# Kernel tuning notes

Measured on AMD Instinct MI355X. Metric: run time of the kernel, lower is better.

The kernel has to match this reference:

```python
import jax, jax.numpy as jnp
import numpy as np

DIM = 768
HEADS = 12
HEAD_DIM = DIM // HEADS
EPS_ATTN = 1e-6
LN_EPS = 1e-5


def _piece_weight():
    # BlockDistanceConv with num_patches_per_side=16, patch_group_size=16 -> 4x4 blocks
    bps = 4
    centers = np.array([[i + 0.5, j + 0.5] for i in range(bps) for j in range(bps)], dtype=np.float32)
    d = np.linalg.norm(centers[:, None, :] - centers[None, :, :], axis=-1)
    mat = np.cos(d / d.max() * np.pi / 4.0)  # 'cos' transform
    mat = mat / mat.sum(axis=0, keepdims=True)
    return jnp.asarray(mat, dtype=jnp.float32)  # [16, 16], out = W @ x over piece channels


def setup_inputs() -> dict:
    key = jax.random.key(0)
    ks = jax.random.split(key, 4)
    B, N, W, C = 128, 16, 16, DIM
    x = jax.random.normal(ks[0], (B, N, W, C), dtype=jnp.float32)
    ln_gamma = jnp.ones((C,), dtype=jnp.float32)
    ln_beta = jnp.zeros((C,), dtype=jnp.float32)
    w_qkv = jax.random.normal(ks[1], (C, 3 * C), dtype=jnp.float32) * (C ** -0.5)
    w_out = jax.random.normal(ks[2], (C, C), dtype=jnp.float32) * (C ** -0.5)
    b_out = jnp.zeros((C,), dtype=jnp.float32)
    w_piece = _piece_weight()
    return {"x": x, "ln_gamma": ln_gamma, "ln_beta": ln_beta, "w_qkv": w_qkv,
            "w_out": w_out, "b_out": b_out, "w_piece": w_piece}


def reference(x, ln_gamma, ln_beta, w_qkv, w_out, b_out, w_piece):
    B, N, W, C = x.shape
    H, D = HEADS, HEAD_DIM
    # LayerNorm over channel dim
    mu = jnp.mean(x, axis=-1, keepdims=True)
    var = jnp.mean((x - mu) ** 2, axis=-1, keepdims=True)
    xn = (x - mu) * jax.lax.rsqrt(var + LN_EPS) * ln_gamma + ln_beta
    # qkv projection (no bias)
    qkv = xn @ w_qkv  # [B,N,W,3C]
    q, k, v = jnp.split(qkv, 3, axis=-1)
    # relu kernel feature map
    q = jax.nn.relu(q) + EPS_ATTN
    k = jax.nn.relu(k) + EPS_ATTN
    # split heads: 'b n w (h d) -> b h n w d'
    def heads(t):
        return t.reshape(B, N, W, H, D).transpose(0, 3, 1, 2, 4)
    q, k, v = heads(q), heads(k), heads(v)
    # per-window kv = k^T v  (sum over window positions w)  -> [B,H,N,D,D]
    kv = jnp.einsum('bhnwd,bhnwe->bhnde', k, v)
    # BlockDistanceConv: 1x1 conv mixing over piece dim N with fixed weights
    kv = jnp.einsum('ij,bhjde->bhide', w_piece, kv)
    # out = q @ kv  -> [B,H,N,W,D]
    out = jnp.einsum('bhnwd,bhnde->bhnwe', q, kv)
    # merge heads: 'b h n w d -> b n w (h d)'
    out = out.transpose(0, 2, 3, 1, 4).reshape(B, N, W, H * D)
    # output projection (dropout is identity in eval)
    return out @ w_out + b_out
```

## Files before the change

### kernel.cpp

```cpp
#include <hip/hip_runtime.h>

#define DIM 768
#define HEADS 12
#define TOK 32768

typedef unsigned short ushort_t;
typedef __attribute__((ext_vector_type(8))) short short8v;
typedef __attribute__((ext_vector_type(4))) float f32x4;
typedef __attribute__((ext_vector_type(4))) unsigned short us4;

__device__ __forceinline__ ushort_t f2bf(float x) {
  union { float f; unsigned u; } c; c.f = x;
  unsigned r = (c.u + 0x7FFFu + ((c.u >> 16) & 1u)) >> 16;
  return (ushort_t)r;
}

__device__ __forceinline__ void gload_lds16(const void* g, void* l) {
  __builtin_amdgcn_global_load_lds((const __attribute__((address_space(1))) void*)g,
                                   (__attribute__((address_space(3))) void*)l, 16, 0, 0);
}

__global__ __launch_bounds__(256) void ln_kernel(const float* __restrict__ x,
                                                 const float* __restrict__ g,
                                                 const float* __restrict__ be,
                                                 ushort_t* __restrict__ xn) {
  int t = blockIdx.x;
  int tid = threadIdx.x;
  const float* row = x + (size_t)t * DIM;
  float v0 = row[tid], v1 = row[tid + 256], v2 = row[tid + 512];
  float s  = v0 + v1 + v2;
  float sq = v0 * v0 + v1 * v1 + v2 * v2;
  #pragma unroll
  for (int off = 32; off; off >>= 1) {
    s  += __shfl_down(s, off);
    sq += __shfl_down(sq, off);
  }
  __shared__ float ls[4], lq[4];
  int wid = tid >> 6, lane = tid & 63;
  if (lane == 0) { ls[wid] = s; lq[wid] = sq; }
  __syncthreads();
  s  = ls[0] + ls[1] + ls[2] + ls[3];
  sq = lq[0] + lq[1] + lq[2] + lq[3];
  float mu  = s * (1.0f / DIM);
  float var = sq * (1.0f / DIM) - mu * mu;
  float rs  = rsqrtf(var + 1e-5f);
  ushort_t* orow = xn + (size_t)t * DIM;
  orow[tid]       = f2bf((v0 - mu) * rs * g[tid]       + be[tid]);
  orow[tid + 256] = f2bf((v1 - mu) * rs * g[tid + 256] + be[tid + 256]);
  orow[tid + 512] = f2bf((v2 - mu) * rs * g[tid + 512] + be[tid + 512]);
}

__global__ __launch_bounds__(256) void convT(const float* __restrict__ src,
                                             ushort_t* __restrict__ dst, int R, int Ccol) {
  __shared__ float tile[32][33];
  int c0 = blockIdx.x * 32, r0 = blockIdx.y * 32;
  int tx = threadIdx.x & 31, ty = threadIdx.x >> 5;
  #pragma unroll
  for (int i = 0; i < 32; i += 8)
    tile[ty + i][tx] = src[(size_t)(r0 + ty + i) * Ccol + c0 + tx];
  __syncthreads();
  #pragma unroll
  for (int i = 0; i < 32; i += 8)
    dst[(size_t)(c0 + ty + i) * R + r0 + tx] = f2bf(tile[tx][ty + i]);
}

template <int MODE>
__global__ __launch_bounds__(512, 2) void gemm_big(const ushort_t* __restrict__ A,
                                                   const ushort_t* __restrict__ Bt,
                                                   ushort_t* __restrict__ qbf,
                                                   ushort_t* __restrict__ kbf,
                                                   ushort_t* __restrict__ vTbf,
                                                   const float* __restrict__ bias,
                                                   float* __restrict__ C) {
  extern __shared__ __align__(16) char lds[];
  const int K = DIM, Kb = DIM * 2;
  const int N = (MODE == 0) ? 3 * DIM : DIM;
  const int nbn = N / 256;
  const int NT = K / 32;

  int bid = blockIdx.x;
  int qd = gridDim.x >> 3;
  int wid = (bid & 7) * qd + (bid >> 3);
  int bm = wid / nbn, bn = wid % nbn;
  int row0 = bm * 256, col0 = bn * 256;
  int t = threadIdx.x;
  int lane = t & 63, wave = t >> 6;
  int wr = wave >> 2, wcol = wave & 3;

  const char* Ag = (const char*)(A + (size_t)row0 * K);
  const char* Bg = (const char*)(Bt + (size_t)col0 * K);

  int o0 = t * 16, o1 = 8192 + t * 16;
  int ra0 = o0 >> 6, ra1 = o1 >> 6;
  int cb0 = (o0 & 63) ^ ((ra0 & 3) << 4);
  int cb1 = (o1 & 63) ^ ((ra1 & 3) << 4);
  size_t ga0 = (size_t)ra0 * Kb + cb0;
  size_t ga1 = (size_t)ra1 * Kb + cb1;

  int fr = lane & 15, fkb = (lane >> 4) << 4;
  int sw = fkb ^ ((fr & 3) << 4);
  int aoff = (wr * 128 + fr) * 64 + sw;
  int boff = 16384 + (wcol * 64 + fr) * 64 + sw;

  #define STAGE(tile, slot)                                            \
    do {                                                               \
      char* sb = lds + ((slot) * 32768);                               \
      size_t kb_ = (size_t)(tile) * 64;                                \
      gload_lds16(Ag + ga0 + kb_, sb + o0);                            \
      gload_lds16(Ag + ga1 + kb_, sb + o1);                            \
      gload_lds16(Bg + ga0 + kb_, sb + 16384 + o0);                    \
      gload_lds16(Bg + ga1 + kb_, sb + 16384 + o1);                    \
    } while (0)

  STAGE(0, 0);
  STAGE(1, 1);

  f32x4 acc[8][4] = {};
  for (int kt = 0; kt < NT; ++kt) {
    if (kt + 2 < NT) {
      STAGE(kt + 2, (kt + 2) & 3);
      asm volatile("s_waitcnt vmcnt(8)" ::: "memory");
    } else if (kt + 2 == NT) {
      asm volatile("s_waitcnt vmcnt(4)" ::: "memory");
    } else {
      asm volatile("s_waitcnt vmcnt(0)" ::: "memory");
    }
    __builtin_amdgcn_s_barrier();
    const char* As = lds + ((kt & 3) * 32768);
    short8v a[8], b[4];
    #pragma unroll
    for (int m = 0; m < 8; ++m) a[m] = *(const short8v*)(As + aoff + m * 1024);
    #pragma unroll
    for (int n = 0; n < 4; ++n) b[n] = *(const short8v*)(As + boff + n * 1024);
    __builtin_amdgcn_s_setprio(1);
    #pragma unroll
    for (int m = 0; m < 8; ++m)
      #pragma unroll
      for (int n = 0; n < 4; ++n)
        acc[m][n] = __builtin_amdgcn_mfma_f32_16x16x32_bf16(a[m], b[n], acc[m][n], 0, 0, 0);
    __builtin_amdgcn_s_setprio(0);
  }
  #undef STAGE

  int rbase = row0 + wr * 128 + ((lane >> 4) << 2);
  int cbase = col0 + wcol * 64 + fr;
  if constexpr (MODE == 0) {
    #pragma unroll
    for (int m = 0; m < 8; ++m) {
      int r0r = rbase + m * 16;
      #pragma unroll
      for (int n = 0; n < 4; ++n) {
        int c = cbase + n * 16;
        if (c < DIM) {
          #pragma unroll
          for (int j = 0; j < 4; ++j)
            qbf[(size_t)(r0r + j) * DIM + c] = f2bf(fmaxf(acc[m][n][j], 0.0f) + 1e-6f);
        } else if (c < 2 * DIM) {
          #pragma unroll
          for (int j = 0; j < 4; ++j)
            kbf[(size_t)(r0r + j) * DIM + (c - DIM)] = f2bf(fmaxf(acc[m][n][j], 0.0f) + 1e-6f);
        } else {
          int ch = c - 2 * DIM;
          int hh = ch >> 6, e = ch & 63;
          int bb = r0r >> 8, rr = r0r & 255;
          us4 pk;
          #pragma unroll
          for (int j = 0; j < 4; ++j) pk[j] = f2bf(acc[m][n][j]);
          *(us4*)&vTbf[((((size_t)bb * HEADS + hh) * 64 + e) << 8) + rr] = pk;
        }
      }
    }
  } else {
    #pragma unroll
    for (int m = 0; m < 8; ++m) {
      #pragma unroll
      for (int n = 0; n < 4; ++n) {
        int c = cbase + n * 16;
        float bz = bias[c];
        #pragma unroll
        for (int j = 0; j < 4; ++j)
          C[(size_t)(rbase + m * 16 + j) * N + c] = acc[m][n][j] + bz;
      }
    }
  }
}

__global__ __launch_bounds__(512) void attn_fused(const ushort_t* __restrict__ qbf,
                                                  const ushort_t* __restrict__ kbf,
                                                  const ushort_t* __restrict__ vTbf,
                                                  const float* __restrict__ wp,
                                                  ushort_t* __restrict__ attnO) {
  __shared__ __align__(16) char lds[65536];
  int bh = blockIdx.x;
  int b = bh / HEADS, h = bh % HEADS;
  int t = threadIdx.x;
  int lane = t & 63, wave = t >> 6;
  int wr = wave >> 2, wc = wave & 3;
  int fr = lane & 15, fkb = (lane >> 4) << 4;

  const char* qg = (const char*)(qbf + ((size_t)b * 256) * DIM + h * 64);
  const char* kg = (const char*)(kbf + ((size_t)b * 256) * DIM + h * 64);
  const char* vg = (const char*)(vTbf + ((size_t)bh << 14));

  for (int q4 = 0; q4 < 4; ++q4) {
    #pragma unroll
    for (int is = 0; is < 4; ++is) {
      int o = is * 8192 + t * 16;
      int r = o >> 7;
      int byt = (o & 127) ^ ((r & 7) << 4);
      gload_lds16(kg + (size_t)r * (DIM * 2) + byt, lds + o);
    }
    {
      int o = t * 16;
      int r = o >> 7;
      int byt = (o & 127) ^ ((r & 7) << 4);
      gload_lds16(qg + (size_t)(q4 * 64 + r) * (DIM * 2) + byt, lds + 32768 + o);
    }
    __syncthreads();
    f32x4 accA[2][4] = {};
    {
      short8v af[2][2], bfv[4][2];
      #pragma unroll
      for (int mt = 0; mt < 2; ++mt)
        #pragma unroll
        for (int ks = 0; ks < 2; ++ks) {
          int r = wr * 32 + mt * 16 + fr;
          int kb = ks * 64 + fkb;
          af[mt][ks] = *(const short8v*)(lds + 32768 + r * 128 + (kb ^ ((r & 7) << 4)));
        }
      #pragma unroll
      for (int nt = 0; nt < 4; ++nt)
        #pragma unroll
        for (int ks = 0; ks < 2; ++ks) {
          int c = wc * 64 + nt * 16 + fr;
          int kb = ks * 64 + fkb;
          bfv[nt][ks] = *(const short8v*)(lds + c * 128 + (kb ^ ((c & 7) << 4)));
        }
      #pragma unroll
      for (int mt = 0; mt < 2; ++mt)
        #pragma unroll
        for (int nt = 0; nt < 4; ++nt)
          #pragma unroll
          for (int ks = 0; ks < 2; ++ks)
            accA[mt][nt] = __builtin_amdgcn_mfma_f32_16x16x32_bf16(af[mt][ks], bfv[nt][ks],
                                                                   accA[mt][nt], 0, 0, 0);
    }
    ushort_t sv[2][4][4];
    #pragma unroll
    for (int mt = 0; mt < 2; ++mt)
      #pragma unroll
      for (int nt = 0; nt < 4; ++nt) {
        float wpf = wp[(q4 * 4 + wr * 2 + mt) * 16 + (wc * 4 + nt)];
        #pragma unroll
        for (int j = 0; j < 4; ++j) sv[mt][nt][j] = f2bf(accA[mt][nt][j] * wpf);
      }
    __syncthreads();
    #pragma unroll
    for (int mt = 0; mt < 2; ++mt)
      #pragma unroll
      for (int nt = 0; nt < 4; ++nt)
        #pragma unroll
        for (int j = 0; j < 4; ++j) {
          int rs = wr * 32 + mt * 16 + ((lane >> 4) << 2) + j;
          int cs = wc * 64 + nt * 16 + fr;
          *(ushort_t*)(lds + 32768 + rs * 512 + ((cs * 2) ^ ((rs & 7) << 4))) = sv[mt][nt][j];
        }
    #pragma unroll
    for (int is = 0; is < 4; ++is) {
      int o = is * 8192 + t * 16;
      int e = o >> 9;
      int byt = (o & 511) ^ ((e & 7) << 4);
      gload_lds16(vg + e * 512 + byt, lds + o);
    }
    __syncthreads();
    f32x4 accB[2] = {{0.f,0.f,0.f,0.f},{0.f,0.f,0.f,0.f}};
    #pragma unroll
    for (int ks = 0; ks < 8; ++ks) {
      int kb = ks * 64 + fkb;
      int e = wc * 16 + fr;
      short8v bv = *(const short8v*)(lds + e * 512 + (kb ^ ((e & 7) << 4)));
      #pragma unroll
      for (int mt = 0; mt < 2; ++mt) {
        int r = wr * 32 + mt * 16 + fr;
        short8v av = *(const short8v*)(lds + 32768 + r * 512 + (kb ^ ((r & 7) << 4)));
        accB[mt] = __builtin_amdgcn_mfma_f32_16x16x32_bf16(av, bv, accB[mt], 0, 0, 0);
      }
    }
    #pragma unroll
    for (int mt = 0; mt < 2; ++mt) {
      int row = b * 256 + q4 * 64 + wr * 32 + mt * 16 + ((lane >> 4) << 2);
      int col = h * 64 + wc * 16 + fr;
      #pragma unroll
      for (int j = 0; j < 4; ++j)
        attnO[(size_t)(row + j) * DIM + col] = f2bf(accB[mt][j]);
    }
    __syncthreads();
  }
}

extern "C" void kernel_launch(void* const* d_in, const int* in_sizes, int n_in,
                              void* d_out, int out_size, void* d_ws, size_t ws_size,
                              hipStream_t stream) {
  const float* x    = (const float*)d_in[0];
  const float* g    = (const float*)d_in[1];
  const float* be   = (const float*)d_in[2];
  const float* wqkv = (const float*)d_in[3];
  const float* wout = (const float*)d_in[4];
  const float* bout = (const float*)d_in[5];
  const float* wp   = (const float*)d_in[6];
  float* out = (float*)d_out;

  char* w = (char*)d_ws;
  const size_t SZ = (size_t)TOK * DIM * 2;
  ushort_t* qbf   = (ushort_t*)(w);
  ushort_t* kbf   = (ushort_t*)(w + SZ);
  ushort_t* vTbf  = (ushort_t*)(w + 2 * SZ);
  ushort_t* xn    = (ushort_t*)(w + 3 * SZ);
  ushort_t* wqkvT = (ushort_t*)(w + 4 * SZ);
  ushort_t* woutT = (ushort_t*)(w + 4 * SZ + 3538944);
  ushort_t* attnO = xn;

  (void)hipFuncSetAttribute(reinterpret_cast<const void*>(&gemm_big<0>),
                            hipFuncAttributeMaxDynamicSharedMemorySize, 131072);
  (void)hipFuncSetAttribute(reinterpret_cast<const void*>(&gemm_big<1>),
                            hipFuncAttributeMaxDynamicSharedMemorySize, 131072);

  dim3 gt1(3 * DIM / 32, DIM / 32);
  convT<<<gt1, 256, 0, stream>>>(wqkv, wqkvT, DIM, 3 * DIM);
  dim3 gt2(DIM / 32, DIM / 32);
  convT<<<gt2, 256, 0, stream>>>(wout, woutT, DIM, DIM);

  ln_kernel<<<TOK, 256, 0, stream>>>(x, g, be, xn);

  gemm_big<0><<<(TOK / 256) * (3 * DIM / 256), 512, 131072, stream>>>(
      xn, wqkvT, qbf, kbf, vTbf, nullptr, nullptr);

  attn_fused<<<128 * HEADS, 512, 0, stream>>>(qbf, kbf, vTbf, wp, attnO);

  gemm_big<1><<<(TOK / 256) * (DIM / 256), 512, 131072, stream>>>(
      attnO, woutT, nullptr, nullptr, nullptr, bout, out);
}
```

Baseline: 321.3 us.

## Rewrite GEMM main loop as 8-phase ping-pong schedule with K=64 tiles

```diff
diff --git a/kernel.cpp b/kernel.cpp
--- a/kernel.cpp
+++ b/kernel.cpp
@@ -65,7 +65,7 @@
 }
 
 template <int MODE>
-__global__ __launch_bounds__(512, 2) void gemm_big(const ushort_t* __restrict__ A,
+__global__ __launch_bounds__(512, 2) void gemm_8ph(const ushort_t* __restrict__ A,
                                                    const ushort_t* __restrict__ Bt,
                                                    ushort_t* __restrict__ qbf,
                                                    ushort_t* __restrict__ kbf,
@@ -76,7 +76,7 @@
   const int K = DIM, Kb = DIM * 2;
   const int N = (MODE == 0) ? 3 * DIM : DIM;
   const int nbn = N / 256;
-  const int NT = K / 32;
+  const size_t GHalf = (size_t)64 * Kb;
 
   int bid = blockIdx.x;
   int qd = gridDim.x >> 3;
@@ -85,65 +85,102 @@
   int row0 = bm * 256, col0 = bn * 256;
   int t = threadIdx.x;
   int lane = t & 63, wave = t >> 6;
-  int wr = wave >> 2, wcol = wave & 3;
-
-  const char* Ag = (const char*)(A + (size_t)row0 * K);
-  const char* Bg = (const char*)(Bt + (size_t)col0 * K);
-
-  int o0 = t * 16, o1 = 8192 + t * 16;
-  int ra0 = o0 >> 6, ra1 = o1 >> 6;
-  int cb0 = (o0 & 63) ^ ((ra0 & 3) << 4);
-  int cb1 = (o1 & 63) ^ ((ra1 & 3) << 4);
-  size_t ga0 = (size_t)ra0 * Kb + cb0;
-  size_t ga1 = (size_t)ra1 * Kb + cb1;
+  int wr = wave >> 2, wc = wave & 3;
+
+  const char* Ag = (const char*)A + (size_t)row0 * Kb;
+  const char* Bg = (const char*)Bt + (size_t)col0 * Kb;
+
+  int o0 = t * 16;
+  int sr = o0 >> 7;
+  int skb = (o0 & 127) ^ ((sr & 7) << 4);
+  size_t goff = (size_t)sr * Kb + skb;
+
+  #define STG(Gbase, Lbase, kt)                                               \
+    do {                                                                      \
+      gload_lds16((Gbase) + goff + (size_t)(kt) * 128, lds + (Lbase) + o0);   \
+      gload_lds16((Gbase) + goff + GHalf + (size_t)(kt) * 128,                \
+                  lds + (Lbase) + o0 + 8192);                                 \
+    } while (0)
 
   int fr = lane & 15, fkb = (lane >> 4) << 4;
-  int sw = fkb ^ ((fr & 3) << 4);
-  int aoff = (wr * 128 + fr) * 64 + sw;
-  int boff = 16384 + (wcol * 64 + fr) * 64 + sw;
-
-  #define STAGE(tile, slot)                                            \
-    do {                                                               \
-      char* sb = lds + ((slot) * 32768);                               \
-      size_t kb_ = (size_t)(tile) * 64;                                \
-      gload_lds16(Ag + ga0 + kb_, sb + o0);                            \
-      gload_lds16(Ag + ga1 + kb_, sb + o1);                            \
-      gload_lds16(Bg + ga0 + kb_, sb + 16384 + o0);                    \
-      gload_lds16(Bg + ga1 + kb_, sb + 16384 + o1);                    \
+  int swz = (fr & 7) << 4;
+  int kb0 = fkb ^ swz;
+  int kb1 = (64 + fkb) ^ swz;
+  int laA = (wr * 128 + fr) * 128;
+  int laB = 32768 + (wc * 64 + fr) * 128;
+
+  #define LOAD_A(dst, dbase, mq)                                              \
+    _Pragma("unroll") for (int mi = 0; mi < 4; ++mi) {                        \
+      dst[mi][0] = *(const short8v*)(lds + (dbase) + laA + (mq)*8192 + mi*2048 + kb0); \
+      dst[mi][1] = *(const short8v*)(lds + (dbase) + laA + (mq)*8192 + mi*2048 + kb1); \
+    }
+  #define LOAD_B(dst, dbase, nq)                                              \
+    _Pragma("unroll") for (int ni = 0; ni < 2; ++ni) {                        \
+      dst[ni][0] = *(const short8v*)(lds + (dbase) + laB + (nq)*4096 + ni*2048 + kb0); \
+      dst[ni][1] = *(const short8v*)(lds + (dbase) + laB + (nq)*4096 + ni*2048 + kb1); \
+    }
+  #define MFMA16(av, bv, mq, nq)                                              \
+    do {                                                                      \
+      __builtin_amdgcn_s_setprio(1);                                          \
+      _Pragma("unroll") for (int mi = 0; mi < 4; ++mi)                        \
+        _Pragma("unroll") for (int ni = 0; ni < 2; ++ni) {                    \
+          acc[(mq)*4+mi][(nq)*2+ni] = __builtin_amdgcn_mfma_f32_16x16x32_bf16(\
+              av[mi][0], bv[ni][0], acc[(mq)*4+mi][(nq)*2+ni], 0, 0, 0);      \
+          acc[(mq)*4+mi][(nq)*2+ni] = __builtin_amdgcn_mfma_f32_16x16x32_bf16(\
+              av[mi][1], bv[ni][1], acc[(mq)*4+mi][(nq)*2+ni], 0, 0, 0);      \
+        }                                                                     \
+      __builtin_amdgcn_s_setprio(0);                                          \
     } while (0)
-
-  STAGE(0, 0);
-  STAGE(1, 1);
+  #define FENCE asm volatile("" ::: "memory")
+  #define BAR do { FENCE; __builtin_amdgcn_s_barrier(); FENCE; } while (0)
+  #define LGK asm volatile("s_waitcnt lgkmcnt(0)" ::: "memory")
+
+  STG(Ag, 0, 0);  STG(Ag + 128 * Kb, 16384, 0);
+  STG(Bg, 32768, 0);  STG(Bg + 128 * Kb, 49152, 0);
+  STG(Ag, 65536, 1);  STG(Ag + 128 * Kb, 65536 + 16384, 1);
+  STG(Bg, 65536 + 32768, 1);
+  asm volatile("s_waitcnt vmcnt(6)" ::: "memory");
+  __builtin_amdgcn_s_barrier();
 
   f32x4 acc[8][4] = {};
-  for (int kt = 0; kt < NT; ++kt) {
-    if (kt + 2 < NT) {
-      STAGE(kt + 2, (kt + 2) & 3);
-      asm volatile("s_waitcnt vmcnt(8)" ::: "memory");
-    } else if (kt + 2 == NT) {
-      asm volatile("s_waitcnt vmcnt(4)" ::: "memory");
-    } else {
-      asm volatile("s_waitcnt vmcnt(0)" ::: "memory");
-    }
-    __builtin_amdgcn_s_barrier();
-    const char* As = lds + ((kt & 3) * 32768);
-    short8v a[8], b[4];
-    #pragma unroll
-    for (int m = 0; m < 8; ++m) a[m] = *(const short8v*)(As + aoff + m * 1024);
-    #pragma unroll
-    for (int n = 0; n < 4; ++n) b[n] = *(const short8v*)(As + boff + n * 1024);
-    __builtin_amdgcn_s_setprio(1);
-    #pragma unroll
-    for (int m = 0; m < 8; ++m)
-      #pragma unroll
-      for (int n = 0; n < 4; ++n)
-        acc[m][n] = __builtin_amdgcn_mfma_f32_16x16x32_bf16(a[m], b[n], acc[m][n], 0, 0, 0);
-    __builtin_amdgcn_s_setprio(0);
+  for (int it = 0; it < 6; ++it) {
+    const int d0 = 0, d1 = 65536;
+    int t1k = 2 * it + 1, t2k = 2 * it + 2, t3k = 2 * it + 3;
+    bool st = (it < 5);
+    short8v ar[4][2], a2[4][2], br[2][2], b2[2][2];
+    LOAD_A(ar, d0, 0); LOAD_B(br, d0, 0);
+    STG(Bg + 128 * Kb, d1 + 49152, t1k);
+    BAR; LGK; MFMA16(ar, br, 0, 0); BAR;
+    LOAD_A(a2, d0, 1);
+    BAR; LGK; MFMA16(a2, br, 1, 0); BAR;
+    LOAD_B(b2, d0, 1);
+    if (st) { STG(Ag, d0, t2k); STG(Ag + 128 * Kb, d0 + 16384, t2k); }
+    BAR; LGK; MFMA16(ar, b2, 0, 1); BAR;
+    if (st) STG(Bg, d0 + 32768, t2k);
+    BAR; LGK; MFMA16(a2, b2, 1, 1);
+    if (st) asm volatile("s_waitcnt vmcnt(6)" ::: "memory");
+    else    asm volatile("s_waitcnt vmcnt(0)" ::: "memory");
+    BAR;
+    LOAD_A(ar, d1, 0); LOAD_B(br, d1, 0);
+    if (st) STG(Bg + 128 * Kb, d0 + 49152, t2k);
+    BAR; LGK; MFMA16(ar, br, 0, 0); BAR;
+    LOAD_A(a2, d1, 1);
+    BAR; LGK; MFMA16(a2, br, 1, 0); BAR;
+    LOAD_B(b2, d1, 1);
+    if (st) { STG(Ag, d1, t3k); STG(Ag + 128 * Kb, d1 + 16384, t3k); }
+    BAR; LGK; MFMA16(ar, b2, 0, 1); BAR;
+    if (st) STG(Bg, d1 + 32768, t3k);
+    BAR; LGK; MFMA16(a2, b2, 1, 1);
+    if (st) asm volatile("s_waitcnt vmcnt(6)" ::: "memory");
+    BAR;
   }
-  #undef STAGE
+  #undef STG
+  #undef LOAD_A
+  #undef LOAD_B
+  #undef MFMA16
 
   int rbase = row0 + wr * 128 + ((lane >> 4) << 2);
-  int cbase = col0 + wcol * 64 + fr;
+  int cbase = col0 + wc * 64 + fr;
   if constexpr (MODE == 0) {
     #pragma unroll
     for (int m = 0; m < 8; ++m) {
@@ -320,9 +357,9 @@
   ushort_t* woutT = (ushort_t*)(w + 4 * SZ + 3538944);
   ushort_t* attnO = xn;
 
-  (void)hipFuncSetAttribute(reinterpret_cast<const void*>(&gemm_big<0>),
+  (void)hipFuncSetAttribute(reinterpret_cast<const void*>(&gemm_8ph<0>),
                             hipFuncAttributeMaxDynamicSharedMemorySize, 131072);
-  (void)hipFuncSetAttribute(reinterpret_cast<const void*>(&gemm_big<1>),
+  (void)hipFuncSetAttribute(reinterpret_cast<const void*>(&gemm_8ph<1>),
                             hipFuncAttributeMaxDynamicSharedMemorySize, 131072);
 
   dim3 gt1(3 * DIM / 32, DIM / 32);
@@ -332,11 +369,11 @@
 
   ln_kernel<<<TOK, 256, 0, stream>>>(x, g, be, xn);
 
-  gemm_big<0><<<(TOK / 256) * (3 * DIM / 256), 512, 131072, stream>>>(
+  gemm_8ph<0><<<(TOK / 256) * (3 * DIM / 256), 512, 131072, stream>>>(
       xn, wqkvT, qbf, kbf, vTbf, nullptr, nullptr);
 
   attn_fused<<<128 * HEADS, 512, 0, stream>>>(qbf, kbf, vTbf, wp, attnO);
 
-  gemm_big<1><<<(TOK / 256) * (DIM / 256), 512, 131072, stream>>>(
+  gemm_8ph<1><<<(TOK / 256) * (DIM / 256), 512, 131072, stream>>>(
       attnO, woutT, nullptr, nullptr, nullptr, bout, out);
 }
```

After: 309.3 us. 3.7% less time.
